# Performance work log

Hardware: AMD Instinct MI355X
Metric: run time of the kernel (lower is better)

## Reference

```python
import jax, jax.numpy as jnp
import numpy as np
import math

D = 768      # embedding_dim
H = 12       # attn_n_heads
HD = D // H  # head_dim = 64
F = 3072     # ff_latent_dim
B, S = 1, 4096
EPS = 1e-5


def setup_inputs() -> dict:
    key = jax.random.key(0)
    ks = jax.random.split(key, 16)
    s = 0.02
    return {
        "x": jax.random.normal(ks[0], (B, S, D), jnp.float32),
        # per-head Q/K/V projections stacked: [H, D, HD]
        "Wq": jax.random.normal(ks[1], (H, D, HD), jnp.float32) * s,
        "bq": jnp.zeros((H, HD), jnp.float32),
        "Wk": jax.random.normal(ks[2], (H, D, HD), jnp.float32) * s,
        "bk": jnp.zeros((H, HD), jnp.float32),
        "Wv": jax.random.normal(ks[3], (H, D, HD), jnp.float32) * s,
        "bv": jnp.zeros((H, HD), jnp.float32),
        "Wo": jax.random.normal(ks[4], (D, D), jnp.float32) * s,
        "bo": jnp.zeros((D,), jnp.float32),
        "ln1_w": jnp.ones((D,), jnp.float32),
        "ln1_b": jnp.zeros((D,), jnp.float32),
        "ln2_w": jnp.ones((D,), jnp.float32),
        "ln2_b": jnp.zeros((D,), jnp.float32),
        "W1": jax.random.normal(ks[5], (D, F), jnp.float32) * s,
        "b1": jnp.zeros((F,), jnp.float32),
        "W2": jax.random.normal(ks[6], (F, D), jnp.float32) * s,
        "b2": jnp.zeros((D,), jnp.float32),
    }


def _layer_norm(z, w, b):
    mu = jnp.mean(z, axis=-1, keepdims=True)
    var = jnp.mean(jnp.square(z - mu), axis=-1, keepdims=True)
    return (z - mu) * jax.lax.rsqrt(var + EPS) * w + b


def reference(x, Wq, bq, Wk, bk, Wv, bv, Wo, bo,
              ln1_w, ln1_b, ln2_w, ln2_b, W1, b1, W2, b2):
    # pre-norm attention block
    y = _layer_norm(x, ln1_w, ln1_b)
    q = jnp.einsum('bsd,hde->bhse', y, Wq) + bq[None, :, None, :]
    k = jnp.einsum('bsd,hde->bhse', y, Wk) + bk[None, :, None, :]
    v = jnp.einsum('bsd,hde->bhse', y, Wv) + bv[None, :, None, :]
    scores = jnp.einsum('bhqe,bhke->bhqk', q, k) * (1.0 / math.sqrt(HD))
    attn = jax.nn.softmax(scores, axis=-1)            # [B,H,S,S]
    o = jnp.einsum('bhqk,bhke->bhqe', attn, v)        # [B,H,S,HD]
    o = o.transpose(0, 2, 1, 3).reshape(x.shape[0], x.shape[1], D)  # concat heads
    o = o @ Wo + bo
    x = x + o
    # pre-norm FFN block (eval mode: dropout is identity)
    y = _layer_norm(x, ln2_w, ln2_b)
    h = jax.nn.gelu(y @ W1 + b1, approximate=False)   # torch F.gelu default = exact erf
    x = x + (h @ W2 + b2)
    return x
```

## Files before the change

kernel.cpp:

```cpp
#include <hip/hip_runtime.h>
#include <stdint.h>

typedef __bf16 bf16;
typedef __bf16 bf16x2 __attribute__((ext_vector_type(2)));
typedef __bf16 bf16x4 __attribute__((ext_vector_type(4)));
typedef __bf16 bf16x8 __attribute__((ext_vector_type(8)));
typedef float f32x4 __attribute__((ext_vector_type(4)));
typedef float f32x16 __attribute__((ext_vector_type(16)));
typedef uint32_t u32;
typedef unsigned int u32x2 __attribute__((ext_vector_type(2)));

#define QSCALE 0.1803368801111137f

__device__ __forceinline__ float fast_exp2(float x) {
#if __has_builtin(__builtin_amdgcn_exp2f)
  return __builtin_amdgcn_exp2f(x);
#else
  return exp2f(x);
#endif
}

__device__ __forceinline__ u32 pack_bf16(float a, float b) {
  bf16x2 v; v[0] = (bf16)a; v[1] = (bf16)b;
  return __builtin_bit_cast(u32, v);
}

__device__ __forceinline__ void permswap32(u32& a, u32& b) {
#if __has_builtin(__builtin_amdgcn_permlane32_swap)
  u32x2 r = __builtin_amdgcn_permlane32_swap(a, b, false, false);
  a = r[0]; b = r[1];
#else
  asm volatile("v_permlane32_swap_b32 %0, %1" : "+v"(a), "+v"(b));
#endif
}

__device__ __forceinline__ void async16(void* lds, const void* g) {
  __builtin_amdgcn_global_load_lds(
      (__attribute__((address_space(1))) uint32_t*)(uintptr_t)g,
      (__attribute__((address_space(3))) uint32_t*)(uint32_t)(uintptr_t)lds,
      16, 0, 0);
}

__device__ __forceinline__ void transpose_body(
    const float* __restrict__ in, bf16* __restrict__ outp, int R, int C,
    int bx, int by, float (*tile)[33], int t)
{
  int bc = bx * 32, br = by * 32;
  int tc = t & 31, tr = t >> 5;
  #pragma unroll
  for (int i = 0; i < 4; i++)
    tile[tr + i * 8][tc] = in[(size_t)(br + tr + i * 8) * C + bc + tc];
  __syncthreads();
  #pragma unroll
  for (int i = 0; i < 4; i++) {
    int c = bc + tr + i * 8;
    outp[(size_t)c * R + br + tc] = (bf16)tile[tc][tr + i * 8];
  }
}

__global__ __launch_bounds__(256) void prep_kernel(
    const float* __restrict__ x,
    const float* __restrict__ ln1w, const float* __restrict__ ln1b,
    const float* __restrict__ Wq, const float* __restrict__ Wk,
    const float* __restrict__ Wv,
    const float* __restrict__ Wo, const float* __restrict__ W1,
    const float* __restrict__ W2,
    const float* __restrict__ bq, const float* __restrict__ bk,
    const float* __restrict__ bv,
    bf16* __restrict__ ybuf, bf16* __restrict__ Wqkv_t,
    bf16* __restrict__ Wo_t, bf16* __restrict__ W1_t, bf16* __restrict__ W2_t,
    float* __restrict__ bqkv)
{
  __shared__ float tile[32][33];
  int n = blockIdx.x;
  int t = threadIdx.x;
  if (n < 4096) {
    int row = n;
    const float* xr = x + (size_t)row * 768;
    float v0 = xr[t], v1 = xr[t + 256], v2 = xr[t + 512];
    float s = v0 + v1 + v2, s2 = v0 * v0 + v1 * v1 + v2 * v2;
    #pragma unroll
    for (int d = 1; d < 64; d <<= 1) {
      s  += __shfl_xor(s, d, 64);
      s2 += __shfl_xor(s2, d, 64);
    }
    float* red = &tile[0][0];
    int wv = t >> 6, ln = t & 63;
    if (ln == 0) { red[wv] = s; red[4 + wv] = s2; }
    __syncthreads();
    s  = red[0] + red[1] + red[2] + red[3];
    s2 = red[4] + red[5] + red[6] + red[7];
    float mu = s * (1.0f / 768.0f);
    float var = s2 * (1.0f / 768.0f) - mu * mu;
    float rstd = rsqrtf(var + 1e-5f);
    bf16* yr = ybuf + (size_t)row * 768;
    yr[t]       = (bf16)((v0 - mu) * rstd * ln1w[t]       + ln1b[t]);
    yr[t + 256] = (bf16)((v1 - mu) * rstd * ln1w[t + 256] + ln1b[t + 256]);
    yr[t + 512] = (bf16)((v2 - mu) * rstd * ln1w[t + 512] + ln1b[t + 512]);
  } else if (n < 5824) {
    int n2 = n - 4096;
    int bz = n2 / 48, rem = n2 - bz * 48;
    int by = rem / 24, bx = rem - by * 24;
    int part = bz / 12, h = bz - part * 12;
    const float* W = (part == 0) ? Wq : (part == 1) ? Wk : Wv;
    float sc = (part == 0) ? QSCALE : 1.0f;
    int bd = bx * 32, be = by * 32;
    int tc = t & 31, tr = t >> 5;
    #pragma unroll
    for (int i = 0; i < 4; i++)
      tile[tr + i * 8][tc] = W[((size_t)h * 768 + bd + tr + i * 8) * 64 + be + tc] * sc;
    __syncthreads();
    #pragma unroll
    for (int i = 0; i < 4; i++) {
      int e = be + tr + i * 8;
      Wqkv_t[(size_t)(part * 768 + h * 64 + e) * 768 + bd + tc] = (bf16)tile[tc][tr + i * 8];
    }
  } else if (n < 6400) {
    int m = n - 5824;
    transpose_body(Wo, Wo_t, 768, 768, m % 24, m / 24, tile, t);
  } else if (n < 8704) {
    int m = n - 6400;
    transpose_body(W1, W1_t, 768, 3072, m % 96, m / 96, tile, t);
  } else if (n < 11008) {
    int m = n - 8704;
    transpose_body(W2, W2_t, 3072, 768, m % 24, m / 24, tile, t);
  } else {
    int idx = (n - 11008) * 256 + t;
    int part = idx / 768, nn = idx - part * 768;
    const float* B = (part == 0) ? bq : (part == 1) ? bk : bv;
    float v = B[nn];
    if (part == 0) v *= QSCALE;
    bqkv[idx] = v;
  }
}

__global__ __launch_bounds__(256) void reduce_add_kernel(
    float* __restrict__ out, const bf16* __restrict__ p)
{
  int i = blockIdx.x * 256 + threadIdx.x;
  float4 o = ((float4*)out)[i];
  bf16x4 v = ((const bf16x4*)p)[i];
  o.x += (float)v[0]; o.y += (float)v[1];
  o.z += (float)v[2]; o.w += (float)v[3];
  ((float4*)out)[i] = o;
}

__global__ __launch_bounds__(256) void ln_add_kernel(
    float* __restrict__ x1, const bf16* __restrict__ p,
    const float* __restrict__ w, const float* __restrict__ b,
    bf16* __restrict__ y)
{
  int row = blockIdx.x;
  float* xr = x1 + (size_t)row * 768;
  const bf16* pr = p + (size_t)row * 768;
  int t = threadIdx.x;
  float v0 = xr[t]       + (float)pr[t];
  float v1 = xr[t + 256] + (float)pr[t + 256];
  float v2 = xr[t + 512] + (float)pr[t + 512];
  xr[t] = v0; xr[t + 256] = v1; xr[t + 512] = v2;
  float s = v0 + v1 + v2, s2 = v0 * v0 + v1 * v1 + v2 * v2;
  #pragma unroll
  for (int d = 1; d < 64; d <<= 1) {
    s  += __shfl_xor(s, d, 64);
    s2 += __shfl_xor(s2, d, 64);
  }
  __shared__ float red[8];
  int wv = t >> 6, ln = t & 63;
  if (ln == 0) { red[wv] = s; red[4 + wv] = s2; }
  __syncthreads();
  s  = red[0] + red[1] + red[2] + red[3];
  s2 = red[4] + red[5] + red[6] + red[7];
  float mu = s * (1.0f / 768.0f);
  float var = s2 * (1.0f / 768.0f) - mu * mu;
  float rstd = rsqrtf(var + 1e-5f);
  bf16* yr = y + (size_t)row * 768;
  yr[t]       = (bf16)((v0 - mu) * rstd * w[t]       + b[t]);
  yr[t + 256] = (bf16)((v1 - mu) * rstd * w[t + 256] + b[t + 256]);
  yr[t + 512] = (bf16)((v2 - mu) * rstd * w[t + 512] + b[t + 512]);
}

template <int MODE>
__global__ __launch_bounds__(256) void gemm_bt(
    const bf16* __restrict__ A, const bf16* __restrict__ Bt,
    const float* __restrict__ bias, const float* __restrict__ res,
    void* __restrict__ outp, void* __restrict__ out2, int M, int N, int K)
{
  __shared__ bf16 As[2 * 128 * 32];
  __shared__ bf16 Bs[2 * 128 * 32];
  int t = threadIdx.x;
  int w = t >> 6, lane = t & 63;
  int quad = lane >> 4, l16 = lane & 15;
  int tile_m = blockIdx.y * 128, tile_n = blockIdx.x * 128;

  int srow = lane >> 2;
  int skb = (lane & 3) * 8;
  const bf16* Ag = A  + (size_t)(tile_m + w * 16 + srow) * K + skb;
  const bf16* Bg = Bt + (size_t)(tile_n + w * 16 + srow) * K + skb;
  char* AsB = (char*)As + w * 1024;
  char* BsB = (char*)Bs + w * 1024;
  size_t rstep = (size_t)64 * K;

  int wm = (w >> 1) * 64, wn = (w & 1) * 64;
  f32x4 acc[4][4] = {};

  int kbeg = 0, kend = K;
  if (MODE == 5) {
    int half = K >> 1;
    kbeg = blockIdx.z * half;
    kend = kbeg + half;
  }

  async16(AsB,        Ag + kbeg);
  async16(AsB + 4096, Ag + rstep + kbeg);
  async16(BsB,        Bg + kbeg);
  async16(BsB + 4096, Bg + rstep + kbeg);

  int cur = 0;
  for (int k0 = kbeg; k0 < kend; k0 += 32) {
    __syncthreads();
    if (k0 + 32 < kend) {
      char* An = AsB + (cur ^ 1) * 8192;
      char* Bn = BsB + (cur ^ 1) * 8192;
      async16(An,        Ag + k0 + 32);
      async16(An + 4096, Ag + rstep + k0 + 32);
      async16(Bn,        Bg + k0 + 32);
      async16(Bn + 4096, Bg + rstep + k0 + 32);
    }
    const bf16* Ab = As + cur * 4096;
    const bf16* Bb = Bs + cur * 4096;

    bf16x8 af[4], bfr[4];
    #pragma unroll
    for (int mb = 0; mb < 4; mb++)
      af[mb] = *(const bf16x8*)(Ab + (wm + mb * 16 + l16) * 32 + quad * 8);
    #pragma unroll
    for (int nb = 0; nb < 4; nb++)
      bfr[nb] = *(const bf16x8*)(Bb + (wn + nb * 16 + l16) * 32 + quad * 8);
    #pragma unroll
    for (int mb = 0; mb < 4; mb++)
      #pragma unroll
      for (int nb = 0; nb < 4; nb++)
        acc[mb][nb] = __builtin_amdgcn_mfma_f32_16x16x32_bf16(
            af[mb], bfr[nb], acc[mb][nb], 0, 0, 0);
    cur ^= 1;
  }

  #pragma unroll
  for (int mb = 0; mb < 4; mb++) {
    #pragma unroll
    for (int nb = 0; nb < 4; nb++) {
      int col = tile_n + wn + nb * 16 + l16;
      int row0 = tile_m + wm + mb * 16 + quad * 4;
      if (MODE == 4) {
        float bc = bias[col];
        if (col < 1536) {
          #pragma unroll
          for (int r = 0; r < 4; r++)
            ((bf16*)outp)[(size_t)(row0 + r) * 1536 + col] =
                (bf16)(acc[mb][nb][r] + bc);
        } else {
          bf16x4 pk;
          #pragma unroll
          for (int r = 0; r < 4; r++) pk[r] = (bf16)(acc[mb][nb][r] + bc);
          *(bf16x4*)((bf16*)out2 + (size_t)(col - 1536) * 4096 + row0) = pk;
        }
      } else if (MODE == 2) {
        float bc = bias[col];
        #pragma unroll
        for (int r = 0; r < 4; r++) {
          size_t idx = (size_t)(row0 + r) * N + col;
          float v = acc[mb][nb][r] + bc;
          float g = 0.5f * v * (1.0f + erff(v * 0.70710678118654752f));
          ((bf16*)outp)[idx] = (bf16)g;
        }
      } else {
        if (blockIdx.z == 0) {
          float bc = bias[col];
          #pragma unroll
          for (int r = 0; r < 4; r++) {
            size_t idx = (size_t)(row0 + r) * N + col;
            ((float*)outp)[idx] = res[idx] + acc[mb][nb][r] + bc;
          }
        } else {
          #pragma unroll
          for (int r = 0; r < 4; r++) {
            size_t idx = (size_t)(row0 + r) * N + col;
            ((bf16*)out2)[idx] = (bf16)acc[mb][nb][r];
          }
        }
      }
    }
  }
}

__global__ __launch_bounds__(256) void flash_kernel(
    const bf16* __restrict__ qk, const bf16* __restrict__ vtg,
    bf16* __restrict__ Opart, float* __restrict__ Lpart)
{
  __shared__ char smem[49152];
  bf16* Qs = (bf16*)smem;
  int t = threadIdx.x, w = t >> 6, lane = t & 63;
  int l32 = lane & 31, hi = lane >> 5;
  int qt = blockIdx.x, h = blockIdx.y, z = blockIdx.z;
  int q0 = qt * 128, kv0 = z * 2048;
  int qsel = w & 1, ksel = w >> 1;
  int qw = qsel * 64, kb = ksel * 32;

  int srow = lane >> 3, scol = ((lane & 7) ^ srow) * 8;

  #pragma unroll
  for (int c = 0; c < 4; c++) {
    const bf16* qg = qk + (size_t)(q0 + c * 32 + w * 8 + srow) * 1536 + h * 64 + scol;
    async16(smem + c * 4096 + w * 1024, qg);
  }

  const bf16* kg = qk + 768 + h * 64 + (size_t)(kv0 + w * 8 + srow) * 1536 + scol;
  const bf16* vg = vtg + (size_t)(h * 64 + w * 8 + srow) * 4096 + kv0 + scol;

  {
    char* kb0 = smem + 16384 + w * 1024;
    char* vb0 = smem + 32768 + w * 1024;
    async16(kb0,        kg);
    async16(kb0 + 4096, kg + (size_t)32 * 1536);
    async16(vb0,        vg);
    async16(vb0 + 4096, vg + (size_t)32 * 4096);
  }
  __syncthreads();

  int qr0 = qw + l32, qr1 = qw + 32 + l32;
  bf16x8 qf0[4], qf1[4];
  #pragma unroll
  for (int ks = 0; ks < 4; ks++) {
    qf0[ks] = *(const bf16x8*)(Qs + qr0 * 64 + (((ks * 2 + hi) ^ (qr0 & 7)) * 8));
    qf1[ks] = *(const bf16x8*)(Qs + qr1 * 64 + (((ks * 2 + hi) ^ (qr1 & 7)) * 8));
  }

  f32x16 oT00 = {}, oT10 = {}, oT01 = {}, oT11 = {};
  float l0 = 0.0f, l1 = 0.0f;
  int krow = kb + l32;
  int er0 = l32, er1 = 32 + l32;

  for (int j = 0; j < 32; j++) {
    int cur = j & 1;
    if (j < 31) {
      const bf16* kgn = kg + (size_t)(j + 1) * 64 * 1536;
      const bf16* vgn = vg + (j + 1) * 64;
      char* kbn = smem + 16384 + (cur ^ 1) * 8192 + w * 1024;
      char* vbn = smem + 32768 + (cur ^ 1) * 8192 + w * 1024;
      async16(kbn,        kgn);
      async16(kbn + 4096, kgn + (size_t)32 * 1536);
      async16(vbn,        vgn);
      async16(vbn + 4096, vgn + (size_t)32 * 4096);
    }
    const bf16* Ks = (const bf16*)(smem + 16384 + cur * 8192);
    const bf16* Vs = (const bf16*)(smem + 32768 + cur * 8192);

    f32x16 s0 = {}, s1 = {};
    __builtin_amdgcn_s_setprio(1);
    #pragma unroll
    for (int ks = 0; ks < 4; ks++) {
      bf16x8 kf = *(const bf16x8*)(Ks + krow * 64 + (((ks * 2 + hi) ^ (krow & 7)) * 8));
      s0 = __builtin_amdgcn_mfma_f32_32x32x16_bf16(kf, qf0[ks], s0, 0, 0, 0);
      s1 = __builtin_amdgcn_mfma_f32_32x32x16_bf16(kf, qf1[ks], s1, 0, 0, 0);
    }
    __builtin_amdgcn_s_setprio(0);

    bf16x8 pf00, pf01, pf10, pf11;
    {
      float p[16];
      #pragma unroll
      for (int i = 0; i < 16; i++) p[i] = fast_exp2(s0[i]);
      float t0 = (p[0] + p[1]) + (p[2] + p[3]);
      float t1 = (p[4] + p[5]) + (p[6] + p[7]);
      float t2 = (p[8] + p[9]) + (p[10] + p[11]);
      float t3 = (p[12] + p[13]) + (p[14] + p[15]);
      l0 += (t0 + t1) + (t2 + t3);
      u32 dd[8];
      #pragma unroll
      for (int k = 0; k < 8; k++) dd[k] = pack_bf16(p[2 * k], p[2 * k + 1]);
      permswap32(dd[0], dd[2]);
      permswap32(dd[1], dd[3]);
      permswap32(dd[4], dd[6]);
      permswap32(dd[5], dd[7]);
      pf00 = __builtin_bit_cast(bf16x8, uint4{dd[0], dd[1], dd[2], dd[3]});
      pf01 = __builtin_bit_cast(bf16x8, uint4{dd[4], dd[5], dd[6], dd[7]});
    }
    {
      float p[16];
      #pragma unroll
      for (int i = 0; i < 16; i++) p[i] = fast_exp2(s1[i]);
      float t0 = (p[0] + p[1]) + (p[2] + p[3]);
      float t1 = (p[4] + p[5]) + (p[6] + p[7]);
      float t2 = (p[8] + p[9]) + (p[10] + p[11]);
      float t3 = (p[12] + p[13]) + (p[14] + p[15]);
      l1 += (t0 + t1) + (t2 + t3);
      u32 dd[8];
      #pragma unroll
      for (int k = 0; k < 8; k++) dd[k] = pack_bf16(p[2 * k], p[2 * k + 1]);
      permswap32(dd[0], dd[2]);
      permswap32(dd[1], dd[3]);
      permswap32(dd[4], dd[6]);
      permswap32(dd[5], dd[7]);
      pf10 = __builtin_bit_cast(bf16x8, uint4{dd[0], dd[1], dd[2], dd[3]});
      pf11 = __builtin_bit_cast(bf16x8, uint4{dd[4], dd[5], dd[6], dd[7]});
    }

    __builtin_amdgcn_s_setprio(1);
    #pragma unroll
    for (int kstep = 0; kstep < 2; kstep++) {
      int grp = (kb >> 3) + kstep * 2 + hi;
      bf16x8 va = *(const bf16x8*)(Vs + er0 * 64 + ((grp ^ (er0 & 7)) * 8));
      bf16x8 vb = *(const bf16x8*)(Vs + er1 * 64 + ((grp ^ (er1 & 7)) * 8));
      bf16x8 pa = kstep ? pf01 : pf00;
      bf16x8 pb = kstep ? pf11 : pf10;
      oT00 = __builtin_amdgcn_mfma_f32_32x32x16_bf16(va, pa, oT00, 0, 0, 0);
      oT10 = __builtin_amdgcn_mfma_f32_32x32x16_bf16(vb, pa, oT10, 0, 0, 0);
      oT01 = __builtin_amdgcn_mfma_f32_32x32x16_bf16(va, pb, oT01, 0, 0, 0);
      oT11 = __builtin_amdgcn_mfma_f32_32x32x16_bf16(vb, pb, oT11, 0, 0, 0);
    }
    __builtin_amdgcn_s_setprio(0);

    __syncthreads();
  }

  float lq0 = l0 + __shfl_xor(l0, 32, 64);
  float lq1 = l1 + __shfl_xor(l1, 32, 64);
  float* OS = (float*)smem;
  float* LS = (float*)(smem + 34304);
  if (ksel == 1) {
    #pragma unroll
    for (int i = 0; i < 16; i++) {
      int eoff = (i & 3) + 8 * (i >> 2) + 4 * hi;
      OS[qr0 * 67 + eoff]      = oT00[i];
      OS[qr0 * 67 + 32 + eoff] = oT10[i];
      OS[qr1 * 67 + eoff]      = oT01[i];
      OS[qr1 * 67 + 32 + eoff] = oT11[i];
    }
    if (hi == 0) { LS[qr0] = lq0; LS[qr1] = lq1; }
  }
  __syncthreads();
  if (ksel == 0) {
    size_t tb = ((size_t)z * 12 + h) * 32 + qt;
    float la0 = lq0 + LS[qr0], la1 = lq1 + LS[qr1];
    if (hi == 0) { Lpart[tb * 128 + qr0] = la0; Lpart[tb * 128 + qr1] = la1; }
    bf16* ob0 = Opart + tb * 8192 + (size_t)qr0 * 64;
    bf16* ob1 = Opart + tb * 8192 + (size_t)qr1 * 64;
    #pragma unroll
    for (int g = 0; g < 4; g++) {
      int e0 = 8 * g + 4 * hi;
      bf16x4 a0, a1, b0, b1;
      #pragma unroll
      for (int r = 0; r < 4; r++) {
        a0[r] = (bf16)(oT00[g * 4 + r] + OS[qr0 * 67 + e0 + r]);
        a1[r] = (bf16)(oT10[g * 4 + r] + OS[qr0 * 67 + 32 + e0 + r]);
        b0[r] = (bf16)(oT01[g * 4 + r] + OS[qr1 * 67 + e0 + r]);
        b1[r] = (bf16)(oT11[g * 4 + r] + OS[qr1 * 67 + 32 + e0 + r]);
      }
      *(bf16x4*)(ob0 + e0)      = a0;
      *(bf16x4*)(ob0 + 32 + e0) = a1;
      *(bf16x4*)(ob1 + e0)      = b0;
      *(bf16x4*)(ob1 + 32 + e0) = b1;
    }
  }
}

__global__ __launch_bounds__(256) void flash_combine_kernel(
    const bf16* __restrict__ Opart, const float* __restrict__ Lpart,
    bf16* __restrict__ o)
{
  int qt = blockIdx.x, h = blockIdx.y;
  int t = threadIdx.x;
  size_t t0 = (size_t)h * 32 + qt;
  size_t t1 = (size_t)(12 + h) * 32 + qt;
  #pragma unroll
  for (int qq = 0; qq < 2; qq++) {
    int q = qq * 64 + (t >> 2), eg = (t & 3) * 16;
    float inv = 1.0f / (Lpart[t0 * 128 + q] + Lpart[t1 * 128 + q]);
    const bf16* p0 = Opart + t0 * 8192 + (size_t)q * 64 + eg;
    const bf16* p1 = Opart + t1 * 8192 + (size_t)q * 64 + eg;
    bf16x8 a0 = *(const bf16x8*)p0, a1 = *(const bf16x8*)(p0 + 8);
    bf16x8 b0 = *(const bf16x8*)p1, b1 = *(const bf16x8*)(p1 + 8);
    bf16x8 r0, r1;
    #pragma unroll
    for (int i = 0; i < 8; i++) {
      r0[i] = (bf16)(((float)a0[i] + (float)b0[i]) * inv);
      r1[i] = (bf16)(((float)a1[i] + (float)b1[i]) * inv);
    }
    bf16* op = o + (size_t)(qt * 128 + q) * 768 + h * 64 + eg;
    *(bf16x8*)op       = r0;
    *(bf16x8*)(op + 8) = r1;
  }
}

extern "C" void kernel_launch(void* const* d_in, const int* in_sizes, int n_in,
                              void* d_out, int out_size, void* d_ws, size_t ws_size,
                              hipStream_t stream) {
  const float* x    = (const float*)d_in[0];
  const float* Wq   = (const float*)d_in[1];
  const float* bq   = (const float*)d_in[2];
  const float* Wk   = (const float*)d_in[3];
  const float* bk   = (const float*)d_in[4];
  const float* Wv   = (const float*)d_in[5];
  const float* bv   = (const float*)d_in[6];
  const float* Wo   = (const float*)d_in[7];
  const float* bo   = (const float*)d_in[8];
  const float* ln1w = (const float*)d_in[9];
  const float* ln1b = (const float*)d_in[10];
  const float* ln2w = (const float*)d_in[11];
  const float* ln2b = (const float*)d_in[12];
  const float* W1   = (const float*)d_in[13];
  const float* b1   = (const float*)d_in[14];
  const float* W2   = (const float*)d_in[15];
  const float* b2   = (const float*)d_in[16];
  float* out = (float*)d_out;

  char* ws = (char*)d_ws;
  bf16*  hbuf   = (bf16*)(ws + 0);
  float* Lpart  = (float*)(ws + 0);
  bf16*  ybuf   = (bf16*)(ws + 0);
  bf16*  qkbuf  = (bf16*)(ws + 6291456);
  bf16*  opar_o = (bf16*)(ws + 6291456);
  bf16*  vtg    = (bf16*)(ws + 18874368);
  float* x1     = (float*)(ws + 25165824);
  bf16*  Opart  = (bf16*)(ws + 25165824);
  bf16*  obuf   = (bf16*)(ws + 37748736);
  bf16*  y2buf  = obuf;
  bf16*  opar_f = obuf;
  bf16*  Wqkv_t = (bf16*)(ws + 44040192);
  bf16*  Wo_t   = (bf16*)(ws + 47579136);
  bf16*  W1_t   = (bf16*)(ws + 48758784);
  bf16*  W2_t   = (bf16*)(ws + 53477376);
  float* bqkv   = (float*)(ws + 58195968);

  prep_kernel<<<11017, 256, 0, stream>>>(x, ln1w, ln1b, Wq, Wk, Wv, Wo, W1, W2,
                                         bq, bk, bv,
                                         ybuf, Wqkv_t, Wo_t, W1_t, W2_t, bqkv);
  gemm_bt<4><<<dim3(18, 32), 256, 0, stream>>>(ybuf, Wqkv_t, bqkv,
                                               (const float*)nullptr, qkbuf, vtg,
                                               4096, 2304, 768);
  flash_kernel<<<dim3(32, 12, 2), 256, 0, stream>>>(qkbuf, vtg, Opart, Lpart);
  flash_combine_kernel<<<dim3(32, 12), 256, 0, stream>>>(Opart, Lpart, obuf);
  gemm_bt<5><<<dim3(6, 32, 2), 256, 0, stream>>>(obuf, Wo_t, bo, x, x1, opar_o,
                                                 4096, 768, 768);
  ln_add_kernel<<<4096, 256, 0, stream>>>(x1, opar_o, ln2w, ln2b, y2buf);
  gemm_bt<2><<<dim3(24, 32), 256, 0, stream>>>(y2buf, W1_t, b1,
                                               (const float*)nullptr, hbuf, nullptr,
                                               4096, 3072, 768);
  gemm_bt<5><<<dim3(6, 32, 2), 256, 0, stream>>>(hbuf, W2_t, b2, x1, out, opar_f,
                                                 4096, 768, 3072);
  reduce_add_kernel<<<3072, 256, 0, stream>>>(out, opar_f);
}
```

Before: 311.0 us.

## Split FFN down-projection K three ways and use a fast erf approximation for GELU

The W2 GEMM now splits its K dimension across three z-slices instead of two. Two bf16 partial buffers are written, and a new reduce kernel adds both into the output. This raises the block count for the 768-wide output GEMM so more compute units stay busy. Separately, the exact erff in the GELU epilogue is replaced with an Abramowitz-Stegun style polynomial that uses hardware exp2 and reciprocal. The polynomial is cheaper but less accurate, and the second partial buffer at a fixed workspace offset risks overlapping other buffers.

```diff
diff --git a/kernel.cpp b/kernel.cpp
--- a/kernel.cpp
+++ b/kernel.cpp
@@ -18,6 +18,25 @@
 #else
   return exp2f(x);
 #endif
+}
+
+__device__ __forceinline__ float fast_rcp(float x) {
+#if __has_builtin(__builtin_amdgcn_rcpf)
+  return __builtin_amdgcn_rcpf(x);
+#else
+  return 1.0f / x;
+#endif
+}
+
+__device__ __forceinline__ float fast_gelu(float v) {
+  float u = v * 0.70710678118654752f;
+  float a = __builtin_fabsf(u);
+  float t = fast_rcp(__builtin_fmaf(0.47047f, a, 1.0f));
+  float e = fast_exp2(-a * a * 1.4426950408889634f);
+  float poly = ((0.7478556f * t - 0.0958798f) * t + 0.3480242f) * t;
+  float erf_abs = __builtin_fmaf(-poly, e, 1.0f);
+  float erf = __builtin_copysignf(erf_abs, u);
+  return 0.5f * v * (1.0f + erf);
 }
 
 __device__ __forceinline__ u32 pack_bf16(float a, float b) {
@@ -134,14 +153,18 @@
   }
 }
 
-__global__ __launch_bounds__(256) void reduce_add_kernel(
-    float* __restrict__ out, const bf16* __restrict__ p)
+__global__ __launch_bounds__(256) void reduce_add2_kernel(
+    float* __restrict__ out, const bf16* __restrict__ p1,
+    const bf16* __restrict__ p2)
 {
   int i = blockIdx.x * 256 + threadIdx.x;
   float4 o = ((float4*)out)[i];
-  bf16x4 v = ((const bf16x4*)p)[i];
-  o.x += (float)v[0]; o.y += (float)v[1];
-  o.z += (float)v[2]; o.w += (float)v[3];
+  bf16x4 a = ((const bf16x4*)p1)[i];
+  bf16x4 b = ((const bf16x4*)p2)[i];
+  o.x += (float)a[0] + (float)b[0];
+  o.y += (float)a[1] + (float)b[1];
+  o.z += (float)a[2] + (float)b[2];
+  o.w += (float)a[3] + (float)b[3];
   ((float4*)out)[i] = o;
 }
 
@@ -205,9 +228,9 @@
 
   int kbeg = 0, kend = K;
   if (MODE == 5) {
-    int half = K >> 1;
-    kbeg = blockIdx.z * half;
-    kend = kbeg + half;
+    int slice = K / (int)gridDim.z;
+    kbeg = blockIdx.z * slice;
+    kend = kbeg + slice;
   }
 
   async16(AsB,        Ag + kbeg);
@@ -269,9 +292,7 @@
         #pragma unroll
         for (int r = 0; r < 4; r++) {
           size_t idx = (size_t)(row0 + r) * N + col;
-          float v = acc[mb][nb][r] + bc;
-          float g = 0.5f * v * (1.0f + erff(v * 0.70710678118654752f));
-          ((bf16*)outp)[idx] = (bf16)g;
+          ((bf16*)outp)[idx] = (bf16)fast_gelu(acc[mb][nb][r] + bc);
         }
       } else {
         if (blockIdx.z == 0) {
@@ -282,10 +303,11 @@
             ((float*)outp)[idx] = res[idx] + acc[mb][nb][r] + bc;
           }
         } else {
+          size_t pbase = (size_t)(blockIdx.z - 1) * M * N;
           #pragma unroll
           for (int r = 0; r < 4; r++) {
             size_t idx = (size_t)(row0 + r) * N + col;
-            ((bf16*)out2)[idx] = (bf16)acc[mb][nb][r];
+            ((bf16*)out2)[pbase + idx] = (bf16)acc[mb][nb][r];
           }
         }
       }
@@ -546,7 +568,8 @@
   gemm_bt<2><<<dim3(24, 32), 256, 0, stream>>>(y2buf, W1_t, b1,
                                                (const float*)nullptr, hbuf, nullptr,
                                                4096, 3072, 768);
-  gemm_bt<5><<<dim3(6, 32, 2), 256, 0, stream>>>(hbuf, W2_t, b2, x1, out, opar_f,
+  gemm_bt<5><<<dim3(6, 32, 3), 256, 0, stream>>>(hbuf, W2_t, b2, x1, out, opar_f,
                                                  4096, 768, 3072);
-  reduce_add_kernel<<<3072, 256, 0, stream>>>(out, opar_f);
-}
+  reduce_add2_kernel<<<3072, 256, 0, stream>>>(out, opar_f,
+                                               (const bf16*)(ws + 44040192));
+}
```

Measured after the change: 315.2 us. Within noise of the previous version (+1.3%).
